# Kernel optimization log

Hardware: AMD Instinct MI355X
Metric: run time of the kernel (lower is better)

The kernel has to match this reference:

```python
import jax, jax.numpy as jnp
import numpy as np

# Plan (mirrors pytorch_ffa's plan.steps rows)
PLAN = [{"dsfactor": 1.0, "bins_min": 128, "bins_max": 132, "tsamp": 0.000064}]

B, C, T = 4, 2, 2097152


def _linear_resize(x, out_len):
    # F.interpolate(mode='linear', align_corners=False) equivalent (no antialias)
    in_len = x.shape[-1]
    if out_len == in_len:
        return x
    scale = in_len / out_len
    src = (jnp.arange(out_len, dtype=jnp.float32) + 0.5) * scale - 0.5
    src = jnp.clip(src, 0.0, in_len - 1)
    lo = jnp.floor(src).astype(jnp.int32)
    hi = jnp.minimum(lo + 1, in_len - 1)
    w = src - lo.astype(jnp.float32)
    return x[..., lo] * (1.0 - w) + x[..., hi] * w


def _groupshiftadd(x, n_row_group):
    # x: [B, C, G, n_row_group, nCol]; vectorized over the row-group loop:
    # y[i] = x[i//2] + roll(x[i//2 + half], (i+1)//2)
    n_col = x.shape[-1]
    half = n_row_group // 2
    i = np.arange(n_row_group)
    iA = i // 2
    iB = iA + half
    Bs = (i + 1) // 2
    # roll by Bs[i] along last axis == gather at (j - Bs[i]) mod nCol
    col = (np.arange(n_col)[None, :] - Bs[:, None]) % n_col  # [n_row_group, nCol]
    xA = x[:, :, :, iA, :]
    xB = jnp.take_along_axis(x[:, :, :, iB, :], jnp.asarray(col)[None, None, None, :, :], axis=4)
    return xA + xB


def _ffa(x):
    # x: [B, C, R, bins] with R a power of two; log2(R) butterfly stages
    b, c, R, n_col = x.shape
    nstage = int(np.log2(R))
    for stage in range(1, nstage + 1):
        g = 2 ** stage
        x = _groupshiftadd(x.reshape(b, c, R // g, g, n_col), g)
        x = x.reshape(b, c, R, n_col)
    return x


def _calc_snr(profiles, added_rows, std_dev):
    # torch.median returns the lower median (sorted index (n-1)//2)
    bins = profiles.shape[3]
    mx = profiles.max(axis=3)
    med = jnp.sort(profiles, axis=3)[..., (bins - 1) // 2]
    return (mx - med) / std_dev[:, :, None] / np.sqrt(profiles.shape[2] - added_rows)


def reference(x):
    std_dev = jnp.std(x, axis=2, ddof=1)  # torch .std() is unbiased
    outs = []
    periods = []
    for step in PLAN:
        out_len = int(x.shape[2] // step["dsfactor"])  # floor(N * 1/scale)
        down = _linear_resize(x, out_len)
        for bins in range(step["bins_min"], step["bins_max"]):
            trunc = down.shape[2] % bins
            p = down[:, :, :down.shape[2] - trunc] if trunc else down
            r = p.reshape(p.shape[0], p.shape[1], -1, bins)
            rows = r.shape[2]
            target = 1 << int(np.ceil(np.log2(rows)))
            added = target - rows
            if added:
                r = jnp.pad(r, ((0, 0), (0, 0), (0, added), (0, 0)))
            ffa_out = _ffa(r)
            outs.append(_calc_snr(ffa_out, added, std_dev))
            p0 = step["tsamp"] * bins
            p1 = step["tsamp"] * (bins + 1)
            periods.append(np.linspace(p0, p1, target))
    return jnp.asarray(np.concatenate(periods), dtype=jnp.float32), jnp.concatenate(outs, axis=2)


def setup_inputs() -> dict:
    key = jax.random.key(0)
    x = jax.random.normal(key, (B, C, T), dtype=jnp.float32)
    return {"x": x}
```

## Files before the change

kernel.cpp:

```cpp
#include <hip/hip_runtime.h>
#include <hip/hip_fp16.h>
#include <math.h>


typedef unsigned int u32;

#define T_LEN   2097152
#define RTOT    16384
#define YSTR    70
#define B_BUF_DW (128 * YSTR)
#define PP_LDS_BYTES (2 * B_BUF_DW * 4)
#define YBIN_DW ((size_t)8 * RTOT * YSTR)

#define WS_PART_OFF 0
#define WS_Y_OFF    33024
#define WS_SERIAL_NEEDED  (33024 + YBIN_DW * 4)
#define WS_MERGED_NEEDED  (33024 + 4 * YBIN_DW * 4)

#define HINF2 0x7C007C00u
#define NINF2 0xFC00FC00u

__device__ __forceinline__ u32 alnp(u32 lo, u32 hi) { return (lo >> 16) | (hi << 16); }
__device__ __forceinline__ __half2 asH2(u32 v) { union { u32 u; __half2 h; } x; x.u = v; return x.h; }
__device__ __forceinline__ u32 asU32(__half2 h) { union { u32 u; __half2 h2; } x; x.h2 = h; return x.u; }
__device__ __forceinline__ u32 hmin2u(u32 a, u32 b) {
  u32 r; asm("v_pk_min_f16 %0, %1, %2" : "=v"(r) : "v"(a), "v"(b)); return r;
}
__device__ __forceinline__ u32 hmax2u(u32 a, u32 b) {
  u32 r; asm("v_pk_max_f16 %0, %1, %2" : "=v"(r) : "v"(a), "v"(b)); return r;
}

__global__ void k_periods(float* __restrict__ out) {
  int i = blockIdx.x * 256 + threadIdx.x;
  int bi = i >> 14, j = i & 16383;
  double tsamp = 6.4e-05;
  double p0 = tsamp * (double)(128 + bi);
  double p1 = tsamp * (double)(129 + bi);
  double step = (p1 - p0) / 16383.0;
  double v = (j == 16383) ? p1 : (p0 + (double)j * step);
  out[i] = (float)v;
}

__device__ __forceinline__ void pair16_col(const u32* r0p, const u32* r1p,
                                           const u32* r2p, const u32* r3p,
                                           int c0, int s1p, int s2p, int s3p,
                                           int ncol, u32 outw[4]) {
  u32 a = r0p[c0 >> 1];
  int q1 = c0 - s1p; if (q1 < 0) q1 += ncol;
  int q2 = c0 - s2p; if (q2 < 0) q2 += ncol;
  int q3 = c0 - s3p; if (q3 < 0) q3 += ncol;
  int b1 = q1 >> 1, o1 = q1 & 1;
  int b2 = q2 >> 1, o2 = q2 & 1;
  int b3 = q3 >> 1, o3 = q3 & 1;
  u32 d10 = r1p[b1], d11 = r1p[b1 + 1];
  u32 d20 = r2p[b2], d21 = r2p[b2 + 1], d22 = r2p[b2 + 2];
  u32 d30 = r3p[b3], d31 = r3p[b3 + 1], d32 = r3p[b3 + 2];
  u32 a1m = alnp(d10, d11);
  u32 a2a = alnp(d20, d21), a2b = alnp(d21, d22);
  u32 a3a = alnp(d30, d31), a3b = alnp(d31, d32);
  u32 V1[2] = { o1 ? a1m : d10,  o1 ? d11 : a1m };
  u32 V2[3] = { o2 ? a2a : d20,  o2 ? d21 : a2a,  o2 ? a2b : d21 };
  u32 V3[4] = { o3 ? a3a : d30,  o3 ? d31 : a3a,  o3 ? a3b : d31,  o3 ? d32 : a3b };
#pragma unroll
  for (int o = 0; o < 4; ++o) {
    int d1 = 1 - (o >> 1);
    int d2 = 2 - ((o + 1) >> 1);
    int d3 = 3 - o;
    __half2 rr = __hadd2(__hadd2(asH2(a), asH2(V1[d1])),
                         __hadd2(asH2(V2[d2]), asH2(V3[d3])));
    outw[o] = asU32(rr);
  }
}

template <int NCOL, int ST, bool BAR>
__device__ __forceinline__ void ffa_pair16(const u32* src, u32* dst, int rextra) {
  int t = threadIdx.x;
  int Q = t >> 5;
  int l = t & 31;
  constexpr int g = 1 << ST;
  int q = Q & ((g >> 1) - 1);
  int B = (Q >> (ST - 1)) << (ST + 1);
  int e1 = (rextra << (ST - 1)) % NCOL;
  int e2m = (rextra << ST) % NCOL;
  int s1 = q + e1; if (s1 >= NCOL) s1 -= NCOL;
  int s2 = 2 * q + e2m; if (s2 >= NCOL) s2 -= NCOL;
  int s3 = s1 + s2; if (s3 >= NCOL) s3 -= NCOL;
  int s1p = s1 + 1; if (s1p >= NCOL) s1p -= NCOL;
  int s2p = s2 + 2; if (s2p >= NCOL) s2p -= NCOL;
  int s3p = s3 + 3; if (s3p >= NCOL) s3p -= NCOL;
  const u32* r0p = src + (size_t)(B + q) * YSTR;
  const u32* r1p = r0p + (size_t)(g >> 1) * YSTR;
  const u32* r2p = r0p + (size_t)g * YSTR;
  const u32* r3p = r2p + (size_t)(g >> 1) * YSTR;

  if constexpr (BAR) __syncthreads();

  u32 outm[2][4];
  pair16_col(r0p, r1p, r2p, r3p, 2 * l,      s1p, s2p, s3p, NCOL, outm[0]);
  pair16_col(r0p, r1p, r2p, r3p, 2 * l + 64, s1p, s2p, s3p, NCOL, outm[1]);
  u32 outt[4];
  bool tact0 = (NCOL > 128) && (l == 0);
  bool tact1 = (NCOL == 131) && (l == 1);
  if (tact0) pair16_col(r0p, r1p, r2p, r3p, 128, s1p, s2p, s3p, NCOL, outt);
  if (tact1) pair16_col(r0p, r1p, r2p, r3p, 130, s1p, s2p, s3p, NCOL, outt);

#pragma unroll
  for (int p = 0; p < 2; ++p)
#pragma unroll
    for (int o = 0; o < 4; ++o)
      dst[(size_t)(B + 4 * q + o) * YSTR + l + 32 * p] = outm[p][o];
  if (l < 3) {
#pragma unroll
    for (int o = 0; o < 4; ++o) {
      __half* hr = (__half*)(dst + (size_t)(B + 4 * q + o) * YSTR);
      __half2 hv = asH2(outm[0][o]);
      hr[NCOL + 2 * l]     = __low2half(hv);
      hr[NCOL + 2 * l + 1] = __high2half(hv);
    }
  }
  if (tact0) {
#pragma unroll
    for (int o = 0; o < 4; ++o) {
      __half* hr = (__half*)(dst + (size_t)(B + 4 * q + o) * YSTR);
      __half2 hv = asH2(outt[o]);
      hr[128] = __low2half(hv);
      if (NCOL > 129) hr[129] = __high2half(hv);
    }
  }
  if (tact1) {
#pragma unroll
    for (int o = 0; o < 4; ++o) {
      __half* hr = (__half*)(dst + (size_t)(B + 4 * q + o) * YSTR);
      hr[130] = __low2half(asH2(outt[o]));
    }
  }
}

template <int NCOL, bool STD>
__device__ __forceinline__ void passA_body(const float* __restrict__ x,
                                           u32* __restrict__ y,
                                           double* __restrict__ part,
                                           int rows_actual,
                                           u32* buf0, u32* buf1, double* sm2) {
  int G = blockIdx.x, bc = blockIdx.y, t = threadIdx.x;
  int w = t >> 6, lane = t & 63;
  const float* src = x + (size_t)bc * T_LEN + (size_t)G * 128 * NCOL;
  double ds = 0.0, ds2 = 0.0;

  if constexpr (NCOL == 128) {
    const float4* src4 = (const float4*)src;
#pragma unroll
    for (int i = 0; i < 4; ++i) {
      int idx = w * 256 + lane + 64 * i;
      float4 v = src4[idx];
      if (STD) {
        ds  += (double)(v.x + v.y + v.z + v.w);
        ds2 += (double)(v.x * v.x + v.y * v.y + v.z * v.z + v.w * v.w);
      }
      int k = idx >> 5, c = (idx & 31) * 4;
      uint2 pk;
      pk.x = asU32(__floats2half2_rn(v.x, v.y));
      pk.y = asU32(__floats2half2_rn(v.z, v.w));
      *(uint2*)(buf0 + k * YSTR + (c >> 1)) = pk;
      if (c < 8) *(uint2*)(buf0 + k * YSTR + 64 + (c >> 1)) = pk;
    }
    (void)rows_actual;
  } else {
    int rowlim = rows_actual - G * 128;
    int lim = rowlim * NCOL;
    __half* hb = (__half*)buf0;
    int base2 = 4 * NCOL * w;
#pragma unroll
    for (int i = 0; i < 9; ++i) {
      int e2 = base2 + lane + 64 * i;
      if (e2 < base2 + 4 * NCOL) {
        int e = e2 * 2;
        float2 v = make_float2(0.f, 0.f);
        if (e + 1 < lim) {
          v = *(const float2*)(src + e);
        } else if (e < lim) {
          v.x = src[e];
        }
        int k = e / NCOL, c = e % NCOL;
        __half h0 = __float2half_rn(v.x), h1 = __float2half_rn(v.y);
        hb[k * 140 + c] = h0;
        if (c < 6) hb[k * 140 + NCOL + c] = h0;
        int k2 = k, c2 = c + 1;
        if (c2 == NCOL) { c2 = 0; ++k2; }
        hb[k2 * 140 + c2] = h1;
        if (c2 < 6) hb[k2 * 140 + NCOL + c2] = h1;
      }
    }
  }
  if (STD) {
    for (int off = 32; off > 0; off >>= 1) {
      ds  += __shfl_down(ds, off);
      ds2 += __shfl_down(ds2, off);
    }
    if (lane == 0) { sm2[w] = ds; sm2[16 + w] = ds2; }
  }

  ffa_pair16<NCOL, 1, false>(buf0, buf1, 0);
  ffa_pair16<NCOL, 3, true >(buf1, buf0, 0);
  ffa_pair16<NCOL, 5, true >(buf0, buf1, 0);
  __syncthreads();

  {
    int p = t >> 4, hh = t & 15;
    const u32* ra = buf1 + (size_t)p * YSTR;
    const u32* rb = buf1 + (size_t)(p + 64) * YSTR;
    u32* dstE = y + ((size_t)bc * RTOT + (size_t)(2 * p) * 128 + G) * YSTR;
    u32* dstO = dstE + (size_t)128 * YSTR;
#pragma unroll
    for (int i = 0; i < 4; ++i) {
      int i0 = hh + 16 * i;
      int j0 = 2 * i0;
      u32 a = ra[i0];
      int qe = j0 - p;  if (qe < 0) qe += NCOL;
      int qo = qe - 1;  if (qo < 0) qo += NCOL;
      u32 be, bo;
      { int bb = qe >> 1; u32 e0 = rb[bb], e1v = rb[bb + 1];
        be = (qe & 1) ? alnp(e0, e1v) : e0; }
      { int bb = qo >> 1; u32 e0 = rb[bb], e1v = rb[bb + 1];
        bo = (qo & 1) ? alnp(e0, e1v) : e0; }
      u32 ve = asU32(__hadd2(asH2(a), asH2(be)));
      u32 vo = asU32(__hadd2(asH2(a), asH2(bo)));
      dstE[i0] = ve;
      dstO[i0] = vo;
      if (i == 0 && hh < 3) {
        __half* hE = (__half*)dstE;
        __half* hO = (__half*)dstO;
        __half2 hve = asH2(ve), hvo = asH2(vo);
        hE[NCOL + j0]     = __low2half(hve);
        hE[NCOL + j0 + 1] = __high2half(hve);
        hO[NCOL + j0]     = __low2half(hvo);
        hO[NCOL + j0 + 1] = __high2half(hvo);
      }
    }
    if (NCOL > 128 && hh == 0) {
      int j0 = 128;
      u32 a = ra[64];
      int qe = j0 - p;
      int qo = qe - 1;
      u32 be, bo;
      { int bb = qe >> 1; u32 e0 = rb[bb], e1v = rb[bb + 1];
        be = (qe & 1) ? alnp(e0, e1v) : e0; }
      { int bb = qo >> 1; u32 e0 = rb[bb], e1v = rb[bb + 1];
        bo = (qo & 1) ? alnp(e0, e1v) : e0; }
      u32 ve = asU32(__hadd2(asH2(a), asH2(be)));
      u32 vo = asU32(__hadd2(asH2(a), asH2(bo)));
      if (NCOL > 129) {
        dstE[64] = ve; dstO[64] = vo;
      } else {
        ((__half*)dstE)[128] = __low2half(asH2(ve));
        ((__half*)dstO)[128] = __low2half(asH2(vo));
      }
    }
    if (NCOL == 131 && hh == 1) {
      int j0 = 130;
      u32 a = ra[65];
      int qe = j0 - p;
      int qo = qe - 1;
      u32 be, bo;
      { int bb = qe >> 1; u32 e0 = rb[bb], e1v = rb[bb + 1];
        be = (qe & 1) ? alnp(e0, e1v) : e0; }
      { int bb = qo >> 1; u32 e0 = rb[bb], e1v = rb[bb + 1];
        bo = (qo & 1) ? alnp(e0, e1v) : e0; }
      ((__half*)dstE)[130] = __low2half(__hadd2(asH2(a), asH2(be)));
      ((__half*)dstO)[130] = __low2half(__hadd2(asH2(a), asH2(bo)));
    }
  }

  if (STD && t == 0) {
    double s = 0.0, s2 = 0.0;
#pragma unroll
    for (int ww = 0; ww < 16; ++ww) { s += sm2[ww]; s2 += sm2[16 + ww]; }
    part[(bc * 128 + G) * 2]     = s;
    part[(bc * 128 + G) * 2 + 1] = s2;
  }
}

template <int NCOL>
__device__ __forceinline__ void passB_body(const u32* __restrict__ y,
                                           const double* __restrict__ part,
                                           float* __restrict__ out,
                                           int added, int bins_idx,
                                           u32* buf0, u32* buf1, float* s_denom) {
  int r = blockIdx.x, bc = blockIdx.y, t = threadIdx.x;
  int w = t >> 6, lane = t & 63;

  if (t < 64) {
    double s  = part[(bc * 128 + t) * 2]     + part[(bc * 128 + t + 64) * 2];
    double s2 = part[(bc * 128 + t) * 2 + 1] + part[(bc * 128 + t + 64) * 2 + 1];
    for (int off = 32; off > 0; off >>= 1) {
      s  += __shfl_down(s, off);
      s2 += __shfl_down(s2, off);
    }
    if (t == 0) {
      double N = (double)T_LEN;
      double var = (s2 - s * s / N) / (N - 1.0);
      *s_denom = (float)(sqrt(var) * sqrt((double)(RTOT - added)));
    }
  }

  const uint4* src4 = (const uint4*)(y + ((size_t)bc * RTOT + (size_t)r * 128) * YSTR);
#pragma unroll
  for (int i = 0; i < 3; ++i) {
    int idx = lane + 64 * i;
    if (idx < 140) *(uint4*)(buf0 + (w * 140 + idx) * 4) = src4[w * 140 + idx];
  }

  ffa_pair16<NCOL, 1, false>(buf0, buf1, r);
  ffa_pair16<NCOL, 3, true >(buf1, buf0, r);
  ffa_pair16<NCOL, 5, true >(buf0, buf1, r);
  __syncthreads();

  int u = t >> 3, h = t & 7;
  int p = u >> 1;
  int extra = (r << 6) % NCOL;
  int s = p + extra; if (s >= NCOL) s -= NCOL;
  s += (u & 1);      if (s >= NCOL) s -= NCOL;
  const u32* ra = buf1 + (size_t)p * YSTR;
  const u32* rb = buf1 + (size_t)(p + 64) * YSTR;
  constexpr int NCHUNK = (NCOL + 3) / 4;
  constexpr int NCK = (NCHUNK + 7) / 8;
  u32 valp[NCK * 2];
  u32 mn2 = HINF2, mx2 = NINF2;
#pragma unroll
  for (int i = 0; i < NCK; ++i) {
    if (NCOL <= 128 || i < 4) {
      int ch = h + 8 * i;
      int j0 = ch * 4;
      uint2 aa = *(const uint2*)(ra + 2 * ch);
      int q0 = j0 - s; if (q0 < 0) q0 += NCOL;
      int bb = q0 >> 1, ob = q0 & 1;
      u32 e0 = rb[bb], e1 = rb[bb + 1], e2 = rb[bb + 2];
      u32 blo = ob ? alnp(e0, e1) : e0;
      u32 bhi = ob ? alnp(e1, e2) : e1;
      u32 v0 = asU32(__hadd2(asH2(aa.x), asH2(blo)));
      u32 v1 = asU32(__hadd2(asH2(aa.y), asH2(bhi)));
      valp[2 * i]     = v0;
      valp[2 * i + 1] = v1;
      mn2 = hmin2u(hmin2u(mn2, v0), v1);
      mx2 = hmax2u(hmax2u(mx2, v0), v1);
    } else {
      if (h == 0) {
        constexpr int j0 = 128;
        uint2 aa = *(const uint2*)(ra + 64);
        int q0 = j0 - s; if (q0 < 0) q0 += NCOL;
        int bb = q0 >> 1, ob = q0 & 1;
        u32 e0 = rb[bb], e1 = rb[bb + 1], e2 = rb[bb + 2];
        u32 blo = ob ? alnp(e0, e1) : e0;
        u32 bhi = ob ? alnp(e1, e2) : e1;
        u32 v0 = asU32(__hadd2(asH2(aa.x), asH2(blo)));
        u32 v1 = asU32(__hadd2(asH2(aa.y), asH2(bhi)));
        u32 v0mn, v1mn, v0mx, v1mx;
        if (NCOL == 129) {
          v0mn = (v0 & 0xFFFFu) | 0x7C000000u; v0mx = (v0 & 0xFFFFu) | 0xFC000000u;
          v1mn = HINF2;                        v1mx = NINF2;
        } else if (NCOL == 130) {
          v0mn = v0;                           v0mx = v0;
          v1mn = HINF2;                        v1mx = NINF2;
        } else {
          v0mn = v0;                           v0mx = v0;
          v1mn = (v1 & 0xFFFFu) | 0x7C000000u; v1mx = (v1 & 0xFFFFu) | 0xFC000000u;
        }
        valp[2 * i]     = v0mn;
        valp[2 * i + 1] = v1mn;
        mn2 = hmin2u(hmin2u(mn2, v0mn), v1mn);
        mx2 = hmax2u(hmax2u(mx2, v0mx), v1mx);
      } else {
        valp[2 * i]     = HINF2;
        valp[2 * i + 1] = HINF2;
      }
    }
  }
#pragma unroll
  for (int off = 1; off < 8; off <<= 1) {
    mn2 = hmin2u(mn2, (u32)__shfl_xor((int)mn2, off));
    mx2 = hmax2u(mx2, (u32)__shfl_xor((int)mx2, off));
  }
  float mn = fminf(__low2float(asH2(mn2)), __high2float(asH2(mn2)));
  float mx = fmaxf(__low2float(asH2(mx2)), __high2float(asH2(mx2)));

  u32* hrow = buf0 + (size_t)u * 68;
  {
    uint4 z = make_uint4(0u, 0u, 0u, 0u);
    *(uint4*)(hrow + h * 8)     = z;
    *(uint4*)(hrow + h * 8 + 4) = z;
  }
  float rng = mx - mn;
  float scale = 128.0f / fmaxf(rng, 1e-30f);
#pragma unroll
  for (int i = 0; i < NCK * 2; ++i) {
    __half2 hv = asH2(valp[i]);
    float f0 = __low2float(hv), f1 = __high2float(hv);
    int b0 = min((int)((f0 - mn) * scale), 127);
    int b1 = min((int)((f1 - mn) * scale), 127);
    atomicAdd(&hrow[b0 >> 1], 1u << ((b0 & 1) * 16));
    atomicAdd(&hrow[b1 >> 1], 1u << ((b1 & 1) * 16));
  }
  int cnt[16];
  {
    uint4 c0v = *(const uint4*)(hrow + h * 8);
    uint4 c1v = *(const uint4*)(hrow + h * 8 + 4);
    u32 wv[8] = {c0v.x, c0v.y, c0v.z, c0v.w, c1v.x, c1v.y, c1v.z, c1v.w};
#pragma unroll
    for (int m = 0; m < 8; ++m) {
      cnt[2 * m]     = (int)(wv[m] & 0xFFFFu);
      cnt[2 * m + 1] = (int)(wv[m] >> 16);
    }
  }
  int local = 0;
#pragma unroll
  for (int i = 0; i < 16; ++i) local += cnt[i];
  int incl = local, tmp;
  tmp = __shfl_up(incl, 1, 8); if (h >= 1) incl += tmp;
  tmp = __shfl_up(incl, 2, 8); if (h >= 2) incl += tmp;
  tmp = __shfl_up(incl, 4, 8); if (h >= 4) incl += tmp;
  int excl = incl - local;
  constexpr int TR = ((NCOL - 1) >> 1) + 1;
  int cum = excl, cross = 0;
#pragma unroll
  for (int i = 0; i < 16; ++i) {
    cum += cnt[i];
    cross += (cum < TR) ? 1 : 0;
  }
  int bcand = (excl < TR && TR <= incl) ? (h * 16 + cross) : (1 << 30);
#pragma unroll
  for (int off = 1; off < 8; off <<= 1)
    bcand = min(bcand, __shfl_xor(bcand, off));

  float med = mn + ((float)bcand + 0.5f) * rng * (1.0f / 128.0f);
  float snr = (mx - med) / (*s_denom);
  if (h == 0)
    out[65536 + (size_t)bc * 65536 + (size_t)bins_idx * RTOT + r * 128 + u] = snr;
}

__global__ __launch_bounds__(1024, 8) void k_passA_m(const float* __restrict__ x,
                                                     u32* __restrict__ y,
                                                     double* __restrict__ part,
                                                     int zbase, int multi) {
  extern __shared__ u32 lds16[];
  __shared__ double sm2[32];
  u32* buf0 = lds16;
  u32* buf1 = lds16 + B_BUF_DW;
  int bi = blockIdx.z + zbase;
  u32* yb = y + (multi ? (size_t)bi * YBIN_DW : 0);
  switch (bi) {
    case 0: passA_body<128, true >(x, yb, part, 16384, buf0, buf1, sm2); break;
    case 1: passA_body<129, false>(x, yb, part, 16256, buf0, buf1, sm2); break;
    case 2: passA_body<130, false>(x, yb, part, 16131, buf0, buf1, sm2); break;
    default: passA_body<131, false>(x, yb, part, 16008, buf0, buf1, sm2); break;
  }
}

__global__ __launch_bounds__(1024, 8) void k_passB_m(const u32* __restrict__ y,
                                                     const double* __restrict__ part,
                                                     float* __restrict__ out,
                                                     int zbase, int multi) {
  extern __shared__ u32 lds16[];
  __shared__ float s_denom;
  u32* buf0 = lds16;
  u32* buf1 = lds16 + B_BUF_DW;
  int bi = blockIdx.z + zbase;
  const u32* yb = y + (multi ? (size_t)bi * YBIN_DW : 0);
  switch (bi) {
    case 0: passB_body<128>(yb, part, out, 0,   0, buf0, buf1, &s_denom); break;
    case 1: passB_body<129>(yb, part, out, 128, 1, buf0, buf1, &s_denom); break;
    case 2: passB_body<130>(yb, part, out, 253, 2, buf0, buf1, &s_denom); break;
    default: passB_body<131>(yb, part, out, 376, 3, buf0, buf1, &s_denom); break;
  }
}

extern "C" void kernel_launch(void* const* d_in, const int* in_sizes, int n_in,
                              void* d_out, int out_size, void* d_ws, size_t ws_size,
                              hipStream_t stream) {
  const float* x = (const float*)d_in[0];
  float* out = (float*)d_out;
  char* ws = (char*)d_ws;
  if (ws_size < WS_SERIAL_NEEDED) return;

  double* part = (double*)(ws + WS_PART_OFF);
  u32*    y    = (u32*)   (ws + WS_Y_OFF);

  (void)hipFuncSetAttribute((const void*)k_passA_m, hipFuncAttributeMaxDynamicSharedMemorySize, PP_LDS_BYTES);
  (void)hipFuncSetAttribute((const void*)k_passB_m, hipFuncAttributeMaxDynamicSharedMemorySize, PP_LDS_BYTES);

  k_periods<<<256, 256, 0, stream>>>(out);

  if (ws_size >= WS_MERGED_NEEDED) {
    k_passA_m<<<dim3(128, 8, 4), 1024, PP_LDS_BYTES, stream>>>(x, y, part, 0, 1);
    k_passB_m<<<dim3(128, 8, 4), 1024, PP_LDS_BYTES, stream>>>(y, part, out, 0, 1);
  } else {
    for (int bi = 0; bi < 4; ++bi) {
      k_passA_m<<<dim3(128, 8, 1), 1024, PP_LDS_BYTES, stream>>>(x, y, part, bi, 0);
      k_passB_m<<<dim3(128, 8, 1), 1024, PP_LDS_BYTES, stream>>>(y, part, out, bi, 0);
    }
  }
}
```

Baseline: 283.5 us.

## Split merged bin kernels into per-bin templated launches reusing one workspace buffer

Replaces the two merged kernels that dispatched on blockIdx.z via a switch with templated kernels launched once per bin size, serialising passA/passB per bin. The intermediate y buffer shrinks to one bin's worth and is reused, so it may stay resident in the last-level cache between the producer and consumer passes. Each kernel is specialised, avoiding register pressure from the union of four bodies. The cost is more kernel launches and lost overlap between bins, plus tail effects per launch.

```diff
diff --git a/kernel.cpp b/kernel.cpp
--- a/kernel.cpp
+++ b/kernel.cpp
@@ -10,12 +10,10 @@
 #define YSTR    70
 #define B_BUF_DW (128 * YSTR)
 #define PP_LDS_BYTES (2 * B_BUF_DW * 4)
-#define YBIN_DW ((size_t)8 * RTOT * YSTR)
 
 #define WS_PART_OFF 0
 #define WS_Y_OFF    33024
-#define WS_SERIAL_NEEDED  (33024 + YBIN_DW * 4)
-#define WS_MERGED_NEEDED  (33024 + 4 * YBIN_DW * 4)
+#define WS_NEEDED   (33024 + (size_t)8 * RTOT * YSTR * 4)
 
 #define HINF2 0x7C007C00u
 #define NINF2 0xFC00FC00u
@@ -137,11 +135,14 @@
 }
 
 template <int NCOL, bool STD>
-__device__ __forceinline__ void passA_body(const float* __restrict__ x,
-                                           u32* __restrict__ y,
-                                           double* __restrict__ part,
-                                           int rows_actual,
-                                           u32* buf0, u32* buf1, double* sm2) {
+__global__ __launch_bounds__(1024, 8) void k_passA(const float* __restrict__ x,
+                                                   u32* __restrict__ y,
+                                                   double* __restrict__ part,
+                                                   int rows_actual) {
+  extern __shared__ u32 lds16[];
+  __shared__ double sm2[32];
+  u32* buf0 = lds16;
+  u32* buf1 = lds16 + B_BUF_DW;
   int G = blockIdx.x, bc = blockIdx.y, t = threadIdx.x;
   int w = t >> 6, lane = t & 63;
   const float* src = x + (size_t)bc * T_LEN + (size_t)G * 128 * NCOL;
@@ -281,11 +282,14 @@
 }
 
 template <int NCOL>
-__device__ __forceinline__ void passB_body(const u32* __restrict__ y,
-                                           const double* __restrict__ part,
-                                           float* __restrict__ out,
-                                           int added, int bins_idx,
-                                           u32* buf0, u32* buf1, float* s_denom) {
+__global__ __launch_bounds__(1024, 8) void k_passB(const u32* __restrict__ y,
+                                                   const double* __restrict__ part,
+                                                   float* __restrict__ out,
+                                                   int added, int bins_idx) {
+  extern __shared__ u32 lds16[];
+  __shared__ float s_denom;
+  u32* buf0 = lds16;
+  u32* buf1 = lds16 + B_BUF_DW;
   int r = blockIdx.x, bc = blockIdx.y, t = threadIdx.x;
   int w = t >> 6, lane = t & 63;
 
@@ -299,7 +303,7 @@
     if (t == 0) {
       double N = (double)T_LEN;
       double var = (s2 - s * s / N) / (N - 1.0);
-      *s_denom = (float)(sqrt(var) * sqrt((double)(RTOT - added)));
+      s_denom = (float)(sqrt(var) * sqrt((double)(RTOT - added)));
     }
   }
 
@@ -432,45 +436,9 @@
     bcand = min(bcand, __shfl_xor(bcand, off));
 
   float med = mn + ((float)bcand + 0.5f) * rng * (1.0f / 128.0f);
-  float snr = (mx - med) / (*s_denom);
+  float snr = (mx - med) / s_denom;
   if (h == 0)
     out[65536 + (size_t)bc * 65536 + (size_t)bins_idx * RTOT + r * 128 + u] = snr;
-}
-
-__global__ __launch_bounds__(1024, 8) void k_passA_m(const float* __restrict__ x,
-                                                     u32* __restrict__ y,
-                                                     double* __restrict__ part,
-                                                     int zbase, int multi) {
-  extern __shared__ u32 lds16[];
-  __shared__ double sm2[32];
-  u32* buf0 = lds16;
-  u32* buf1 = lds16 + B_BUF_DW;
-  int bi = blockIdx.z + zbase;
-  u32* yb = y + (multi ? (size_t)bi * YBIN_DW : 0);
-  switch (bi) {
-    case 0: passA_body<128, true >(x, yb, part, 16384, buf0, buf1, sm2); break;
-    case 1: passA_body<129, false>(x, yb, part, 16256, buf0, buf1, sm2); break;
-    case 2: passA_body<130, false>(x, yb, part, 16131, buf0, buf1, sm2); break;
-    default: passA_body<131, false>(x, yb, part, 16008, buf0, buf1, sm2); break;
-  }
-}
-
-__global__ __launch_bounds__(1024, 8) void k_passB_m(const u32* __restrict__ y,
-                                                     const double* __restrict__ part,
-                                                     float* __restrict__ out,
-                                                     int zbase, int multi) {
-  extern __shared__ u32 lds16[];
-  __shared__ float s_denom;
-  u32* buf0 = lds16;
-  u32* buf1 = lds16 + B_BUF_DW;
-  int bi = blockIdx.z + zbase;
-  const u32* yb = y + (multi ? (size_t)bi * YBIN_DW : 0);
-  switch (bi) {
-    case 0: passB_body<128>(yb, part, out, 0,   0, buf0, buf1, &s_denom); break;
-    case 1: passB_body<129>(yb, part, out, 128, 1, buf0, buf1, &s_denom); break;
-    case 2: passB_body<130>(yb, part, out, 253, 2, buf0, buf1, &s_denom); break;
-    default: passB_body<131>(yb, part, out, 376, 3, buf0, buf1, &s_denom); break;
-  }
 }
 
 extern "C" void kernel_launch(void* const* d_in, const int* in_sizes, int n_in,
@@ -479,23 +447,28 @@
   const float* x = (const float*)d_in[0];
   float* out = (float*)d_out;
   char* ws = (char*)d_ws;
-  if (ws_size < WS_SERIAL_NEEDED) return;
+  if (ws_size < WS_NEEDED) return;
 
   double* part = (double*)(ws + WS_PART_OFF);
   u32*    y    = (u32*)   (ws + WS_Y_OFF);
 
-  (void)hipFuncSetAttribute((const void*)k_passA_m, hipFuncAttributeMaxDynamicSharedMemorySize, PP_LDS_BYTES);
-  (void)hipFuncSetAttribute((const void*)k_passB_m, hipFuncAttributeMaxDynamicSharedMemorySize, PP_LDS_BYTES);
+  (void)hipFuncSetAttribute((const void*)k_passA<128, true>,  hipFuncAttributeMaxDynamicSharedMemorySize, PP_LDS_BYTES);
+  (void)hipFuncSetAttribute((const void*)k_passA<129, false>, hipFuncAttributeMaxDynamicSharedMemorySize, PP_LDS_BYTES);
+  (void)hipFuncSetAttribute((const void*)k_passA<130, false>, hipFuncAttributeMaxDynamicSharedMemorySize, PP_LDS_BYTES);
+  (void)hipFuncSetAttribute((const void*)k_passA<131, false>, hipFuncAttributeMaxDynamicSharedMemorySize, PP_LDS_BYTES);
+  (void)hipFuncSetAttribute((const void*)k_passB<128>, hipFuncAttributeMaxDynamicSharedMemorySize, PP_LDS_BYTES);
+  (void)hipFuncSetAttribute((const void*)k_passB<129>, hipFuncAttributeMaxDynamicSharedMemorySize, PP_LDS_BYTES);
+  (void)hipFuncSetAttribute((const void*)k_passB<130>, hipFuncAttributeMaxDynamicSharedMemorySize, PP_LDS_BYTES);
+  (void)hipFuncSetAttribute((const void*)k_passB<131>, hipFuncAttributeMaxDynamicSharedMemorySize, PP_LDS_BYTES);
 
   k_periods<<<256, 256, 0, stream>>>(out);
 
-  if (ws_size >= WS_MERGED_NEEDED) {
-    k_passA_m<<<dim3(128, 8, 4), 1024, PP_LDS_BYTES, stream>>>(x, y, part, 0, 1);
-    k_passB_m<<<dim3(128, 8, 4), 1024, PP_LDS_BYTES, stream>>>(y, part, out, 0, 1);
-  } else {
-    for (int bi = 0; bi < 4; ++bi) {
-      k_passA_m<<<dim3(128, 8, 1), 1024, PP_LDS_BYTES, stream>>>(x, y, part, bi, 0);
-      k_passB_m<<<dim3(128, 8, 1), 1024, PP_LDS_BYTES, stream>>>(y, part, out, bi, 0);
-    }
-  }
-}
+  k_passA<128, true><<<dim3(128, 8), 1024, PP_LDS_BYTES, stream>>>(x, y, part, 16384);
+  k_passB<128><<<dim3(128, 8), 1024, PP_LDS_BYTES, stream>>>(y, part, out, 0, 0);
+  k_passA<129, false><<<dim3(128, 8), 1024, PP_LDS_BYTES, stream>>>(x, y, part, 16256);
+  k_passB<129><<<dim3(128, 8), 1024, PP_LDS_BYTES, stream>>>(y, part, out, 128, 1);
+  k_passA<130, false><<<dim3(128, 8), 1024, PP_LDS_BYTES, stream>>>(x, y, part, 16131);
+  k_passB<130><<<dim3(128, 8), 1024, PP_LDS_BYTES, stream>>>(y, part, out, 253, 2);
+  k_passA<131, false><<<dim3(128, 8), 1024, PP_LDS_BYTES, stream>>>(x, y, part, 16008);
+  k_passB<131><<<dim3(128, 8), 1024, PP_LDS_BYTES, stream>>>(y, part, out, 376, 3);
+}
```

Result: slower. 322.9 us (+13.9%).
